# Performance work log

Measured on AMD Instinct MI355X. Metric: run time of the kernel, lower is better.

## Reference

```python
import jax, jax.numpy as jnp
from jax import lax
import numpy as np

EMBED = 1024
HIDDEN = 1024
VOCAB = 32000
T = 64


def setup_inputs() -> dict:
    key = jax.random.key(0)
    ks = jax.random.split(key, 8)
    s = 0.02  # weight init scale
    return {
        "captions": jax.random.randint(ks[0], (T,), 0, VOCAB, dtype=jnp.int32),
        "features": jax.random.normal(ks[1], (EMBED,), dtype=jnp.float32),
        "embed_table": jax.random.normal(ks[2], (VOCAB, EMBED), dtype=jnp.float32) * s,
        "W_ih": jax.random.normal(ks[3], (4 * HIDDEN, EMBED), dtype=jnp.float32) * s,
        "W_hh": jax.random.normal(ks[4], (4 * HIDDEN, HIDDEN), dtype=jnp.float32) * s,
        "b_ih": jnp.zeros((4 * HIDDEN,), dtype=jnp.float32),
        "b_hh": jnp.zeros((4 * HIDDEN,), dtype=jnp.float32),
        "fc_W": jax.random.normal(ks[5], (VOCAB, HIDDEN), dtype=jnp.float32) * s,
        "fc_b": jnp.zeros((VOCAB,), dtype=jnp.float32),
    }


def reference(captions, features, embed_table, W_ih, W_hh, b_ih, b_hh, fc_W, fc_b):
    # Embedding lookup for all caption tokens: [T, E]
    emb = embed_table[captions]
    # Input at t=0 is the visual feature; at t>0 it is embed(captions[t-1]).
    xs = jnp.concatenate([features[None, :], emb[:-1]], axis=0)  # [T, E]
    H = W_hh.shape[1]
    bias = b_ih + b_hh  # fuse the two LSTMCell biases

    def step(carry, x):
        h, c = carry  # [H], [H]  (batch = 1, kept 1-D)
        gates = x @ W_ih.T + h @ W_hh.T + bias  # [4H]
        i, f, g, o = jnp.split(gates, 4)  # PyTorch gate order: i, f, g, o
        i = jax.nn.sigmoid(i)
        f = jax.nn.sigmoid(f)
        g = jnp.tanh(g)
        o = jax.nn.sigmoid(o)
        c = f * c + i * g
        h = o * jnp.tanh(c)
        return (h, c), h

    h0 = jnp.zeros((H,), dtype=features.dtype)
    (_, _), hs = lax.scan(step, (h0, h0), xs)  # hs: [T, H]
    # Per-step Linear, expressed as one batched GEMM over all timesteps.
    logits = hs @ fc_W.T + fc_b  # [T, V]
    return logits[None, :, :]  # [1, T, V] to match outputs[:, t, :]
```

## Files before the change

### kernel.cpp

```cpp
#include <hip/hip_runtime.h>
#include <math.h>

#define EMBED  1024
#define HIDDEN 1024
#define VOCAB  32000
#define TSTEPS 64
#define NBLK   256

__global__ __launch_bounds__(256, 1) void decoder_fused(
    const int*   __restrict__ caps,
    const float* __restrict__ feat,
    const float* __restrict__ table,
    const float* __restrict__ Wih,
    const float* __restrict__ Whh,
    const float* __restrict__ bih,
    const float* __restrict__ bhh,
    const float* __restrict__ fcW,
    const float* __restrict__ fcb,
    unsigned long long* hs_pk,
    float* __restrict__ out)
{
    __shared__ __align__(16) char arena[52224];
    __shared__ float xg_s[TSTEPS][16];
    __shared__ float h_s[2][HIDDEN];
    __shared__ int   caps_s[TSTEPS];

    int tid = threadIdx.x;
    int b   = blockIdx.x;

    int lane = tid & 63;
    int wv   = tid >> 6;
    int g    = lane >> 4;
    int c16  = lane & 15;
    int hj   = 4 * b + wv;
    const float4* wrow = (const float4*)(Whh + ((size_t)g * HIDDEN + hj) * HIDDEN);
    float4 wreg[16];
#pragma unroll
    for (int k = 0; k < 16; ++k) wreg[k] = wrow[c16 + 16 * k];

    if (tid < TSTEPS) caps_s[tid] = caps[tid];

    {
        float (*xs_s)[132] = (float (*)[132])arena;
        float (*w16)[132]  = (float (*)[132])(arena + 33792);
        int jl = tid & 15;
        int tg = tid >> 4;
        float acc4[4] = {0.f, 0.f, 0.f, 0.f};
        __syncthreads();

        for (int c = 0; c < 8; ++c) {
            __syncthreads();
            for (int idx = tid; idx < 64 * 32; idx += 256) {
                int r = idx >> 5, f4 = idx & 31;
                const float* src = (r == 0)
                    ? (feat + c * 128)
                    : (table + (size_t)caps_s[r - 1] * EMBED + c * 128);
                *((float4*)&xs_s[r][f4 * 4]) = ((const float4*)src)[f4];
            }
            for (int idx = tid; idx < 16 * 32; idx += 256) {
                int r = idx >> 5, f4 = idx & 31;
                int jr = (r >> 2) * HIDDEN + 4 * b + (r & 3);
                *((float4*)&w16[r][f4 * 4]) =
                    ((const float4*)(Wih + (size_t)jr * EMBED + c * 128))[f4];
            }
            __syncthreads();
            for (int f4 = 0; f4 < 32; ++f4) {
                float4 w = *((const float4*)&w16[jl][f4 * 4]);
#pragma unroll
                for (int k = 0; k < 4; ++k) {
                    float4 x4 = *((const float4*)&xs_s[tg * 4 + k][f4 * 4]);
                    acc4[k] += w.x * x4.x + w.y * x4.y + w.z * x4.z + w.w * x4.w;
                }
            }
        }
        int jrow = (jl >> 2) * HIDDEN + 4 * b + (jl & 3);
        float bias = bih[jrow] + bhh[jrow];
#pragma unroll
        for (int k = 0; k < 4; ++k) xg_s[tg * 4 + k][jl] = acc4[k] + bias;
        __syncthreads();
    }

    float cstate = 0.f;
    for (int t = 0; t < TSTEPS; ++t) {
        float* dst = h_s[t & 1];
        if (t == 0) {
            for (int i = tid; i < HIDDEN; i += 256) dst[i] = 0.f;
        } else {
            const unsigned long long* hsrc = hs_pk + (size_t)(t - 1) * HIDDEN;
            unsigned want = (unsigned)t;
            unsigned long long x0, x1, x2, x3;
            for (;;) {
                x0 = __hip_atomic_load(hsrc + tid, __ATOMIC_RELAXED,
                                       __HIP_MEMORY_SCOPE_AGENT);
                x1 = __hip_atomic_load(hsrc + tid + 256, __ATOMIC_RELAXED,
                                       __HIP_MEMORY_SCOPE_AGENT);
                x2 = __hip_atomic_load(hsrc + tid + 512, __ATOMIC_RELAXED,
                                       __HIP_MEMORY_SCOPE_AGENT);
                x3 = __hip_atomic_load(hsrc + tid + 768, __ATOMIC_RELAXED,
                                       __HIP_MEMORY_SCOPE_AGENT);
                bool ok = ((unsigned)(x0 >> 32) == want) &
                          ((unsigned)(x1 >> 32) == want) &
                          ((unsigned)(x2 >> 32) == want) &
                          ((unsigned)(x3 >> 32) == want);
                if (ok) break;
                __builtin_amdgcn_s_sleep(1);
            }
            dst[tid]       = __uint_as_float((unsigned)x0);
            dst[tid + 256] = __uint_as_float((unsigned)x1);
            dst[tid + 512] = __uint_as_float((unsigned)x2);
            dst[tid + 768] = __uint_as_float((unsigned)x3);
        }
        __syncthreads();

        float4 a = {0.f, 0.f, 0.f, 0.f};
#pragma unroll
        for (int k = 0; k < 16; ++k) {
            float4 w = wreg[k];
            const float* hv = &dst[(c16 + 16 * k) * 4];
            a.x += w.x * hv[0];
            a.y += w.y * hv[1];
            a.z += w.z * hv[2];
            a.w += w.w * hv[3];
        }
        float sum = (a.x + a.y) + (a.z + a.w);
        sum += __shfl_xor(sum, 1);
        sum += __shfl_xor(sum, 2);
        sum += __shfl_xor(sum, 4);
        sum += __shfl_xor(sum, 8);
        float s0 = __shfl(sum, 0);
        float s1 = __shfl(sum, 16);
        float s2 = __shfl(sum, 32);
        float s3 = __shfl(sum, 48);

        if (lane == 0) {
            float gi = s0 + xg_s[t][wv];
            float gf = s1 + xg_s[t][4 + wv];
            float gg = s2 + xg_s[t][8 + wv];
            float go = s3 + xg_s[t][12 + wv];
            float i_ = 1.f / (1.f + expf(-gi));
            float f_ = 1.f / (1.f + expf(-gf));
            float g_ = tanhf(gg);
            float o_ = 1.f / (1.f + expf(-go));
            cstate = f_ * cstate + i_ * g_;
            float hv = o_ * tanhf(cstate);
            unsigned long long pk =
                ((unsigned long long)(unsigned)(t + 1) << 32) |
                (unsigned long long)__float_as_uint(hv);
            __hip_atomic_store(hs_pk + (size_t)t * HIDDEN + hj, pk,
                               __ATOMIC_RELAXED, __HIP_MEMORY_SCOPE_AGENT);
        }
    }
    __syncthreads();

    if (b >= 250) return;
    float (*hs_s)[68] = (float (*)[68])arena;
    float (*w3)[68]   = (float (*)[68])(arena + 17408);
    int tv = tid & 15;
    int tq = tid >> 4;
    int j0 = tv * 4;
    int i0 = tq * 4;
    int v0 = b * 128;
    float acc[4][8];
#pragma unroll
    for (int i = 0; i < 4; ++i)
#pragma unroll
        for (int j = 0; j < 8; ++j) acc[i][j] = 0.f;

    int jcol  = tid & 63;
    int tbase = tid >> 6;

    for (int kc = 0; kc < 16; ++kc) {
        __syncthreads();
        {
            unsigned long long v[16];
            const unsigned long long* src = hs_pk + kc * 64 + jcol;
            for (;;) {
#pragma unroll
                for (int i = 0; i < 16; ++i)
                    v[i] = __hip_atomic_load(src + (size_t)(tbase + 4 * i) * HIDDEN,
                                             __ATOMIC_RELAXED,
                                             __HIP_MEMORY_SCOPE_AGENT);
                bool ok = true;
#pragma unroll
                for (int i = 0; i < 16; ++i)
                    ok &= ((unsigned)(v[i] >> 32) == (unsigned)(tbase + 4 * i + 1));
                if (ok) break;
                __builtin_amdgcn_s_sleep(8);
            }
#pragma unroll
            for (int i = 0; i < 16; ++i)
                hs_s[tbase + 4 * i][jcol] = __uint_as_float((unsigned)v[i]);
        }
#pragma unroll
        for (int i = 0; i < 8; ++i) {
            int idx = tid + i * 256;
            int r = idx >> 4, f4 = idx & 15;
            *((float4*)&w3[r][f4 * 4]) =
                ((const float4*)(fcW + (size_t)(v0 + r) * HIDDEN + kc * 64))[f4];
        }
        __syncthreads();
        for (int q = 0; q < 16; ++q) {
            float4 hv4[4];
#pragma unroll
            for (int i = 0; i < 4; ++i)
                hv4[i] = *((const float4*)&hs_s[i0 + i][q * 4]);
#pragma unroll
            for (int jh = 0; jh < 2; ++jh) {
#pragma unroll
                for (int j = 0; j < 4; ++j) {
                    float4 w4 = *((const float4*)&w3[jh * 64 + j0 + j][q * 4]);
#pragma unroll
                    for (int i = 0; i < 4; ++i) {
                        acc[i][jh * 4 + j] += w4.x * hv4[i].x + w4.y * hv4[i].y +
                                              w4.z * hv4[i].z + w4.w * hv4[i].w;
                    }
                }
            }
        }
    }
#pragma unroll
    for (int jh = 0; jh < 2; ++jh) {
        float b0 = fcb[v0 + jh * 64 + j0 + 0];
        float b1 = fcb[v0 + jh * 64 + j0 + 1];
        float b2 = fcb[v0 + jh * 64 + j0 + 2];
        float b3 = fcb[v0 + jh * 64 + j0 + 3];
#pragma unroll
        for (int i = 0; i < 4; ++i) {
            float4 o = {acc[i][jh * 4 + 0] + b0, acc[i][jh * 4 + 1] + b1,
                        acc[i][jh * 4 + 2] + b2, acc[i][jh * 4 + 3] + b3};
            *((float4*)&out[(size_t)(i0 + i) * VOCAB + v0 + jh * 64 + j0]) = o;
        }
    }
}

extern "C" void kernel_launch(void* const* d_in, const int* in_sizes, int n_in,
                              void* d_out, int out_size, void* d_ws, size_t ws_size,
                              hipStream_t stream) {
    const int*   caps  = (const int*)  d_in[0];
    const float* feat  = (const float*)d_in[1];
    const float* table = (const float*)d_in[2];
    const float* Wih   = (const float*)d_in[3];
    const float* Whh   = (const float*)d_in[4];
    const float* bih   = (const float*)d_in[5];
    const float* bhh   = (const float*)d_in[6];
    const float* fcW   = (const float*)d_in[7];
    const float* fcb   = (const float*)d_in[8];
    float* out = (float*)d_out;

    unsigned long long* hs_pk = (unsigned long long*)d_ws;

    decoder_fused<<<NBLK, 256, 0, stream>>>(caps, feat, table, Wih, Whh,
                                            bih, bhh, fcW, fcb, hs_pk, out);
}
```

Before: 653.6 us.

## Prefetch next fc_W chunk into registers and remap vocab columns to avoid LDS conflicts

```diff
diff --git a/kernel.cpp b/kernel.cpp
--- a/kernel.cpp
+++ b/kernel.cpp
@@ -157,7 +157,6 @@
     float (*w3)[68]   = (float (*)[68])(arena + 17408);
     int tv = tid & 15;
     int tq = tid >> 4;
-    int j0 = tv * 4;
     int i0 = tq * 4;
     int v0 = b * 128;
     float acc[4][8];
@@ -169,10 +168,17 @@
     int jcol  = tid & 63;
     int tbase = tid >> 6;
 
+    float4 wf[8];
+#pragma unroll
+    for (int i = 0; i < 8; ++i) {
+        int idx = tid + i * 256;
+        int r = idx >> 4, f4 = idx & 15;
+        wf[i] = ((const float4*)(fcW + (size_t)(v0 + r) * HIDDEN))[f4];
+    }
+
     for (int kc = 0; kc < 16; ++kc) {
-        __syncthreads();
+        unsigned long long v[16];
         {
-            unsigned long long v[16];
             const unsigned long long* src = hs_pk + kc * 64 + jcol;
             for (;;) {
 #pragma unroll
@@ -187,49 +193,49 @@
                 if (ok) break;
                 __builtin_amdgcn_s_sleep(8);
             }
-#pragma unroll
-            for (int i = 0; i < 16; ++i)
-                hs_s[tbase + 4 * i][jcol] = __uint_as_float((unsigned)v[i]);
-        }
+        }
+        __syncthreads();
 #pragma unroll
         for (int i = 0; i < 8; ++i) {
             int idx = tid + i * 256;
             int r = idx >> 4, f4 = idx & 15;
-            *((float4*)&w3[r][f4 * 4]) =
-                ((const float4*)(fcW + (size_t)(v0 + r) * HIDDEN + kc * 64))[f4];
-        }
-        __syncthreads();
+            *((float4*)&w3[r][f4 * 4]) = wf[i];
+        }
+#pragma unroll
+        for (int i = 0; i < 16; ++i)
+            hs_s[tbase + 4 * i][jcol] = __uint_as_float((unsigned)v[i]);
+        __syncthreads();
+        if (kc < 15) {
+#pragma unroll
+            for (int i = 0; i < 8; ++i) {
+                int idx = tid + i * 256;
+                int r = idx >> 4, f4 = idx & 15;
+                wf[i] = ((const float4*)(fcW + (size_t)(v0 + r) * HIDDEN +
+                                         (kc + 1) * 64))[f4];
+            }
+        }
         for (int q = 0; q < 16; ++q) {
             float4 hv4[4];
 #pragma unroll
             for (int i = 0; i < 4; ++i)
                 hv4[i] = *((const float4*)&hs_s[i0 + i][q * 4]);
 #pragma unroll
-            for (int jh = 0; jh < 2; ++jh) {
-#pragma unroll
-                for (int j = 0; j < 4; ++j) {
-                    float4 w4 = *((const float4*)&w3[jh * 64 + j0 + j][q * 4]);
-#pragma unroll
-                    for (int i = 0; i < 4; ++i) {
-                        acc[i][jh * 4 + j] += w4.x * hv4[i].x + w4.y * hv4[i].y +
-                                              w4.z * hv4[i].z + w4.w * hv4[i].w;
-                    }
+            for (int j = 0; j < 8; ++j) {
+                float4 w4 = *((const float4*)&w3[tv + 16 * j][q * 4]);
+#pragma unroll
+                for (int i = 0; i < 4; ++i) {
+                    acc[i][j] += w4.x * hv4[i].x + w4.y * hv4[i].y +
+                                 w4.z * hv4[i].z + w4.w * hv4[i].w;
                 }
             }
         }
     }
 #pragma unroll
-    for (int jh = 0; jh < 2; ++jh) {
-        float b0 = fcb[v0 + jh * 64 + j0 + 0];
-        float b1 = fcb[v0 + jh * 64 + j0 + 1];
-        float b2 = fcb[v0 + jh * 64 + j0 + 2];
-        float b3 = fcb[v0 + jh * 64 + j0 + 3];
-#pragma unroll
-        for (int i = 0; i < 4; ++i) {
-            float4 o = {acc[i][jh * 4 + 0] + b0, acc[i][jh * 4 + 1] + b1,
-                        acc[i][jh * 4 + 2] + b2, acc[i][jh * 4 + 3] + b3};
-            *((float4*)&out[(size_t)(i0 + i) * VOCAB + v0 + jh * 64 + j0]) = o;
-        }
+    for (int j = 0; j < 8; ++j) {
+        float bj = fcb[v0 + tv + 16 * j];
+#pragma unroll
+        for (int i = 0; i < 4; ++i)
+            out[(size_t)(i0 + i) * VOCAB + v0 + tv + 16 * j] = acc[i][j] + bj;
     }
 }
 
```

Result: slower. 679.5 us (+4.0%).
